# Performance work log

Measured on AMD Instinct MI355X. Metric: run time of the kernel, lower is better.

## Reference

```python
import jax, jax.numpy as jnp
import numpy as np

B, T, W_IN = 64, 512, 40
KS = 3
N = KS * KS          # 9 sampling points
CF = 8               # conv filters
GH = 32              # GRU hidden
GIN = (W_IN - KS + 1) * CF  # 304
ATTN = 32


def setup_inputs() -> dict:
    key = jax.random.key(0)
    ks = jax.random.split(key, 10)
    p = {}
    p["x"] = jax.random.normal(ks[0], (B, 1, T, W_IN), jnp.float32)
    p["p_w"] = jax.random.normal(ks[1], (2 * N, 1, KS, KS), jnp.float32) * 0.01
    p["p_b"] = jnp.zeros((2 * N,), jnp.float32)
    p["dcn_w"] = jax.random.normal(ks[2], (CF, 1, KS, KS), jnp.float32) * 0.1
    p["dcn_b"] = jnp.zeros((CF,), jnp.float32)
    p["w_ih"] = jax.random.normal(ks[3], (3 * GH, GIN), jnp.float32) * 0.05
    p["w_hh"] = jax.random.normal(ks[4], (3 * GH, GH), jnp.float32) * 0.05
    p["b_ih"] = jnp.zeros((3 * GH,), jnp.float32)
    p["b_hh"] = jnp.zeros((3 * GH,), jnp.float32)
    p["w1"] = jax.random.normal(ks[5], (ATTN, GH), jnp.float32) * 0.1
    p["b1"] = jnp.zeros((ATTN,), jnp.float32)
    p["w2"] = jax.random.normal(ks[6], (GH, ATTN), jnp.float32) * 0.1
    p["b2"] = jnp.zeros((GH,), jnp.float32)
    p["w3"] = jax.random.normal(ks[7], (2, GH), jnp.float32) * 0.1
    p["b3"] = jnp.zeros((2,), jnp.float32)
    return p


def _deform_conv(x, p_w, p_b, w, b):
    # x: (B,1,H,W). Deform-conv v1: offsets from a VALID 3x3 conv, bilinear gather.
    Bb, C, H, W = x.shape
    offset = jax.lax.conv_general_dilated(
        x, p_w, (1, 1), "VALID",
        dimension_numbers=("NCHW", "OIHW", "NCHW")) + p_b[None, :, None, None]
    h, w_ = offset.shape[2], offset.shape[3]  # (T-2, 38)
    r = KS // 2
    pny, pnx = jnp.meshgrid(jnp.arange(-r, r + 1), jnp.arange(-r, r + 1), indexing="ij")
    p0y, p0x = jnp.meshgrid(jnp.arange(1, h + 1), jnp.arange(1, w_ + 1), indexing="ij")
    py = offset[:, :N] + pny.reshape(1, N, 1, 1) + p0y[None, None]  # (B,N,h,w)
    px = offset[:, N:] + pnx.reshape(1, N, 1, 1) + p0x[None, None]
    py = jnp.clip(py, 0.0, H - 1.0)
    px = jnp.clip(px, 0.0, W - 1.0)
    y0 = jnp.floor(py).astype(jnp.int32)
    x0 = jnp.floor(px).astype(jnp.int32)
    y1 = jnp.minimum(y0 + 1, H - 1)
    x1 = jnp.minimum(x0 + 1, W - 1)
    wy = (py - y0)[:, None]  # (B,1,N,h,w)
    wx = (px - x0)[:, None]
    flat = x.reshape(Bb, C, H * W)

    def gather(yi, xi):
        idx = (yi * W + xi).reshape(Bb, 1, -1)
        g = jnp.take_along_axis(flat, idx, axis=2)
        return g.reshape(Bb, C, N, h, w_)

    g00 = gather(y0, x0); g01 = gather(y0, x1)
    g10 = gather(y1, x0); g11 = gather(y1, x1)
    samp = (g00 * (1 - wy) * (1 - wx) + g01 * (1 - wy) * wx
            + g10 * wy * (1 - wx) + g11 * wy * wx)  # (B,C,N,h,w)
    out = jnp.einsum("bcnhw,ocn->bohw", samp, w.reshape(w.shape[0], C, N))
    return out + b[None, :, None, None]


def _gru(seq, w_ih, w_hh, b_ih, b_hh):
    # seq: (T,B,GIN); PyTorch GRU equations, single layer, h0 = 0
    xp = jnp.einsum("tbi,hi->tbh", seq, w_ih) + b_ih  # (T,B,3H)
    h0 = jnp.zeros((seq.shape[1], GH), seq.dtype)

    def step(hprev, xt):
        hp = hprev @ w_hh.T + b_hh
        xr, xz, xn = jnp.split(xt, 3, axis=-1)
        hr, hz, hn = jnp.split(hp, 3, axis=-1)
        rg = jax.nn.sigmoid(xr + hr)
        zg = jax.nn.sigmoid(xz + hz)
        ng = jnp.tanh(xn + rg * hn)
        hnew = (1 - zg) * ng + zg * hprev
        return hnew, hnew

    _, ys = jax.lax.scan(step, h0, xp)
    return ys  # (T,B,GH)


def _forward(x, p_w, p_b, dcn_w, dcn_b, w_ih, w_hh, b_ih, b_hh, w1, b1, w2, b2, w3, b3):
    y = _deform_conv(x, p_w, p_b, dcn_w, dcn_b)        # (B,CF,h,w)
    h = y.shape[2]
    y = jnp.transpose(y, (2, 0, 3, 1)).reshape(h, y.shape[1], -1)  # wait
    return y


def _model(x, p_w, p_b, dcn_w, dcn_b, w_ih, w_hh, b_ih, b_hh, w1, b1, w2, b2, w3, b3):
    y = _deform_conv(x, p_w, p_b, dcn_w, dcn_b)        # (B,CF,h,w)
    Bb = y.shape[0]
    h = y.shape[2]
    seq = jnp.transpose(y, (2, 0, 3, 1)).reshape(h, Bb, -1)  # (h,B,w*CF) w-major then channel
    enc = jnp.transpose(_gru(seq, w_ih, w_hh, b_ih, b_hh), (1, 0, 2))  # (B,h,GH)
    a = jnp.tanh(enc @ w1.T + b1) @ w2.T + b2          # (B,h,GH)
    a = jax.nn.softmax(a, axis=1)                      # softmax over time
    pooled = jnp.sum(a * enc, axis=1)                  # (B,GH)
    return pooled @ w3.T + b3                          # (B,2)


def reference(x, p_w, p_b, dcn_w, dcn_b, w_ih, w_hh, b_ih, b_hh, w1, b1, w2, b2, w3, b3):
    return _model(x, p_w, p_b, dcn_w, dcn_b, w_ih, w_hh, b_ih, b_hh, w1, b1, w2, b2, w3, b3)
```

## Files before the change

kernel.cpp:

```cpp
#include <hip/hip_runtime.h>
#include <math.h>
#include <stdint.h>

#define BB 64
#define TT 512
#define W_IN 40
#define CF 8
#define GH 32
#define HOUT 510
#define WOUT 38
#define GIN 304
#define G3 96
#define ATT 32
#define MROWS (HOUT * BB)
#define KC2 152
#define WI_C 19

#define LOG2E 1.4426950408889634f

__device__ __forceinline__ float fast_rcp(float x) {
#if defined(__has_builtin)
# if __has_builtin(__builtin_amdgcn_rcpf)
    return __builtin_amdgcn_rcpf(x);
# else
    return 1.f / x;
# endif
#else
    return 1.f / x;
#endif
}

__device__ __forceinline__ float fast_exp2(float x) {
#if defined(__has_builtin)
# if __has_builtin(__builtin_amdgcn_exp2f)
    return __builtin_amdgcn_exp2f(x);
# else
    return exp2f(x);
# endif
#else
    return exp2f(x);
#endif
}

typedef __attribute__((address_space(3))) uint32_t lds_u32_t;
typedef const __attribute__((address_space(1))) uint32_t glb_u32_t;

__global__ __launch_bounds__(192, 1) void k_dcn_gemm(
    const float* __restrict__ x, const float* __restrict__ p_w, const float* __restrict__ p_b,
    const float* __restrict__ dcn_w, const float* __restrict__ dcn_b,
    const float* __restrict__ w_ih, const float* __restrict__ b_ih,
    float* __restrict__ xp)
{
    __shared__ float As[128 * KC2];
    __shared__ float Ws[96 * KC2];
    __shared__ float pw_s[162], pb_s[18], dw_s[72], db_s[8];

    const int tid = threadIdx.x;
    const int t0  = blockIdx.x * 2;
    const int r0  = blockIdx.x * 128;
    const int mg  = tid / 12;
    const int ng  = tid % 12;

    if (tid < 162) pw_s[tid] = p_w[tid];
    if (tid < 18)  pb_s[tid] = p_b[tid];
    if (tid < 72)  dw_s[tid] = dcn_w[tid];
    if (tid < 8)   db_s[tid] = dcn_b[tid];

    float bih[8];
    #pragma unroll
    for (int j = 0; j < 8; ++j) bih[j] = b_ih[ng + 12 * j];

    float acc[8][8];
    #pragma unroll
    for (int i = 0; i < 8; ++i)
        #pragma unroll
        for (int j = 0; j < 8; ++j) acc[i][j] = 0.f;

    auto stageW = [&](int ch) {
        for (int u4 = tid; u4 < 96 * (KC2 / 4); u4 += 192) {
            const int g   = u4 / (KC2 / 4);
            const int k4l = u4 % (KC2 / 4);
            const float* src = w_ih + (size_t)g * GIN + ch * KC2 + k4l * 4;
            float* dst = &Ws[u4 * 4];
#if defined(__has_builtin) && __has_builtin(__builtin_amdgcn_global_load_lds)
            __builtin_amdgcn_global_load_lds((glb_u32_t*)(uintptr_t)src,
                                             (lds_u32_t*)(uintptr_t)dst, 16, 0, 0);
#else
            *(float4*)dst = *(const float4*)src;
#endif
        }
    };

    auto phaseA = [&](int ch) {
        for (int item = tid; item < 128 * WI_C; item += 192) {
            const int lr = item / WI_C;
            const int wl = item % WI_C;
            const int wi = ch * WI_C + wl;
            const int t  = t0 + (lr >> 6);
            const int b  = lr & 63;
            const float* xb = x + (size_t)b * TT * W_IN;

            float patch[9];
            #pragma unroll
            for (int ky = 0; ky < 3; ++ky)
                #pragma unroll
                for (int kx = 0; kx < 3; ++kx)
                    patch[ky * 3 + kx] = xb[(t + ky) * W_IN + wi + kx];

            float offs[18];
            #pragma unroll
            for (int n = 0; n < 18; ++n) {
                float a = pb_s[n];
                #pragma unroll
                for (int k = 0; k < 9; ++k) a += patch[k] * pw_s[n * 9 + k];
                offs[n] = a;
            }

            float samp[9];
            #pragma unroll
            for (int n = 0; n < 9; ++n) {
                float py = offs[n]     + (float)(n / 3 - 1) + (float)(t + 1);
                float px = offs[9 + n] + (float)(n % 3 - 1) + (float)(wi + 1);
                py = fminf(fmaxf(py, 0.f), (float)(TT - 1));
                px = fminf(fmaxf(px, 0.f), (float)(W_IN - 1));
                float fy = floorf(py), fx = floorf(px);
                int y0 = (int)fy, x0 = (int)fx;
                int y1 = min(y0 + 1, TT - 1), x1 = min(x0 + 1, W_IN - 1);
                float wy = py - fy, wx = px - fx;
                float g00 = xb[y0 * W_IN + x0], g01 = xb[y0 * W_IN + x1];
                float g10 = xb[y1 * W_IN + x0], g11 = xb[y1 * W_IN + x1];
                samp[n] = g00 * (1.f - wy) * (1.f - wx) + g01 * (1.f - wy) * wx
                        + g10 * wy * (1.f - wx) + g11 * wy * wx;
            }

            float o[CF];
            #pragma unroll
            for (int c = 0; c < CF; ++c) {
                float a = db_s[c];
                #pragma unroll
                for (int n = 0; n < 9; ++n) a += samp[n] * dw_s[c * 9 + n];
                o[c] = a;
            }
            float* arow = &As[lr * KC2 + wl * 8];
            ((float4*)arow)[0] = make_float4(o[0], o[1], o[2], o[3]);
            ((float4*)arow)[1] = make_float4(o[4], o[5], o[6], o[7]);
        }
    };

    auto gemm = [&]() {
        #pragma unroll 2
        for (int k4 = 0; k4 < KC2 / 4; ++k4) {
            float4 a[8], w[8];
            #pragma unroll
            for (int i = 0; i < 8; ++i)
                a[i] = *(const float4*)&As[(mg + 16 * i) * KC2 + k4 * 4];
            #pragma unroll
            for (int j = 0; j < 8; ++j)
                w[j] = *(const float4*)&Ws[(ng + 12 * j) * KC2 + k4 * 4];
            #pragma unroll
            for (int i = 0; i < 8; ++i)
                #pragma unroll
                for (int j = 0; j < 8; ++j)
                    acc[i][j] += a[i].x * w[j].x + a[i].y * w[j].y
                               + a[i].z * w[j].z + a[i].w * w[j].w;
        }
    };

    __syncthreads();
    stageW(0);
    phaseA(0);
    __syncthreads();
    gemm();
    __syncthreads();
    stageW(1);
    phaseA(1);
    __syncthreads();
    gemm();

    #pragma unroll
    for (int i = 0; i < 8; ++i) {
        const int row = r0 + mg + 16 * i;
        #pragma unroll
        for (int j = 0; j < 8; ++j)
            xp[(size_t)row * G3 + ng + 12 * j] = acc[i][j] + bih[j];
    }
}

__global__ __launch_bounds__(64) void k_gru(
    const float* __restrict__ xp, const float* __restrict__ w_hh,
    const float* __restrict__ b_hh, float* __restrict__ enc)
{
    const int l = threadIdx.x;
    const int half = l >> 5;
    const int j = l & 31;
    const int b = blockIdx.x;

    float wr[16], wz[16], wn[16];
    #pragma unroll
    for (int i = 0; i < 16; ++i) {
        wr[i] = w_hh[(size_t)j * GH + half * 16 + i];
        wz[i] = w_hh[(size_t)(GH + j) * GH + half * 16 + i];
        wn[i] = w_hh[(size_t)(2 * GH + j) * GH + half * 16 + i];
    }
    const float br = b_hh[j], bz = b_hh[GH + j], bn = b_hh[2 * GH + j];

    float h = 0.f;
    const float* xb = xp + (size_t)b * G3;
    float xr = xb[j], xz = xb[GH + j], xn = xb[2 * GH + j];

    for (int t = 0; t < HOUT; ++t) {
        const int tn = (t + 1 < HOUT) ? t + 1 : t;
        const float* xq = xp + ((size_t)tn * BB + b) * G3;
        float nxr = xq[j], nxz = xq[GH + j], nxn = xq[2 * GH + j];

        float pr = 0.f, pz = 0.f, pn = 0.f;
        #pragma unroll
        for (int i = 0; i < 16; ++i) {
            float hk = __shfl(h, half * 16 + i, 64);
            pr += wr[i] * hk; pz += wz[i] * hk; pn += wn[i] * hk;
        }
        float ar = br + pr + __shfl_xor(pr, 32, 64);
        float az = bz + pz + __shfl_xor(pz, 32, 64);
        float an = bn + pn + __shfl_xor(pn, 32, 64);

        float rg = fast_rcp(1.f + fast_exp2(-(xr + ar) * LOG2E));
        float zg = fast_rcp(1.f + fast_exp2(-(xz + az) * LOG2E));
        float pre = xn + rg * an;
        float e2 = fast_exp2(pre * (2.f * LOG2E));
        float tg = 1.f - 2.f * fast_rcp(e2 + 1.f);
        h = (1.f - zg) * tg + zg * h;

        if (!half) enc[((size_t)b * HOUT + t) * GH + j] = h;
        xr = nxr; xz = nxz; xn = nxn;
    }
}

__global__ __launch_bounds__(256) void k_attn_part(
    const float* __restrict__ enc,
    const float* __restrict__ w1, const float* __restrict__ b1,
    const float* __restrict__ w2, const float* __restrict__ b2,
    float* __restrict__ part)
{
    __shared__ float w1s[ATT * 33], w2s[GH * 33];
    __shared__ float b1s[ATT], b2s[GH];
    __shared__ float encs[8][GH], apres[8][ATT];
    __shared__ float rm[8 * GH], rs[8 * GH], rp[8 * GH];

    const int b   = blockIdx.x >> 2;
    const int c   = blockIdx.x & 3;
    const int tid = threadIdx.x;
    const int ttl = tid >> 5;
    const int j   = tid & 31;

    for (int i = tid; i < ATT * GH; i += 256) {
        int r = i >> 5, cc = i & 31;
        w1s[r * 33 + cc] = w1[i];
        w2s[r * 33 + cc] = w2[i];
    }
    if (tid < ATT)           b1s[tid] = b1[tid];
    else if (tid < ATT + GH) b2s[tid - ATT] = b2[tid - ATT];
    __syncthreads();

    const int tbeg = c * 128;
    const int tend = min(HOUT, tbeg + 128);

    float m = -INFINITY, s = 0.f, p = 0.f;
    const float* encb = enc + (size_t)b * HOUT * GH;

    for (int t0 = tbeg; t0 < tend; t0 += 8) {
        const int t = t0 + ttl;
        const bool act = (t < tend);
        const float ev = act ? encb[t * GH + j] : 0.f;
        encs[ttl][j] = ev;
        __syncthreads();

        float a1 = b1s[j];
        #pragma unroll
        for (int k = 0; k < GH; ++k) a1 += encs[ttl][k] * w1s[j * 33 + k];
        apres[ttl][j] = tanhf(a1);
        __syncthreads();

        float a2 = b2s[j];
        #pragma unroll
        for (int k = 0; k < ATT; ++k) a2 += apres[ttl][k] * w2s[j * 33 + k];

        if (act) {
            float mn = fmaxf(m, a2);
            float sc = expf(m - mn);
            float e  = expf(a2 - mn);
            s = s * sc + e;
            p = p * sc + e * ev;
            m = mn;
        }
        __syncthreads();
    }

    rm[tid] = m; rs[tid] = s; rp[tid] = p;
    __syncthreads();

    if (tid < GH) {
        float M = -INFINITY;
        #pragma unroll
        for (int q = 0; q < 8; ++q) M = fmaxf(M, rm[q * GH + tid]);
        float S = 0.f, P = 0.f;
        #pragma unroll
        for (int q = 0; q < 8; ++q) {
            float sc = expf(rm[q * GH + tid] - M);
            S += rs[q * GH + tid] * sc;
            P += rp[q * GH + tid] * sc;
        }
        float* pb = part + ((size_t)b * 4 + c) * 96;
        pb[tid] = M; pb[32 + tid] = S; pb[64 + tid] = P;
    }
}

__global__ __launch_bounds__(64) void k_attn_fin(
    const float* __restrict__ part,
    const float* __restrict__ w3, const float* __restrict__ b3,
    float* __restrict__ out)
{
    __shared__ float pooled[GH];
    const int b = blockIdx.x;
    const int tid = threadIdx.x;

    if (tid < GH) {
        const float* pb = part + (size_t)b * 4 * 96;
        float M = -INFINITY;
        #pragma unroll
        for (int c = 0; c < 4; ++c) M = fmaxf(M, pb[c * 96 + tid]);
        float S = 0.f, P = 0.f;
        #pragma unroll
        for (int c = 0; c < 4; ++c) {
            float sc = expf(pb[c * 96 + tid] - M);
            S += pb[c * 96 + 32 + tid] * sc;
            P += pb[c * 96 + 64 + tid] * sc;
        }
        pooled[tid] = P / S;
    }
    __syncthreads();

    if (tid < 2) {
        float a = b3[tid];
        #pragma unroll
        for (int k = 0; k < GH; ++k) a += pooled[k] * w3[tid * GH + k];
        out[b * 2 + tid] = a;
    }
}

extern "C" void kernel_launch(void* const* d_in, const int* in_sizes, int n_in,
                              void* d_out, int out_size, void* d_ws, size_t ws_size,
                              hipStream_t stream)
{
    const float* x     = (const float*)d_in[0];
    const float* p_w   = (const float*)d_in[1];
    const float* p_b   = (const float*)d_in[2];
    const float* dcn_w = (const float*)d_in[3];
    const float* dcn_b = (const float*)d_in[4];
    const float* w_ih  = (const float*)d_in[5];
    const float* w_hh  = (const float*)d_in[6];
    const float* b_ih  = (const float*)d_in[7];
    const float* b_hh  = (const float*)d_in[8];
    const float* w1    = (const float*)d_in[9];
    const float* b1    = (const float*)d_in[10];
    const float* w2    = (const float*)d_in[11];
    const float* b2    = (const float*)d_in[12];
    const float* w3    = (const float*)d_in[13];
    const float* b3    = (const float*)d_in[14];
    float* out = (float*)d_out;

    float* xp   = (float*)d_ws;
    float* enc  = xp + (size_t)MROWS * G3;
    float* part = xp;

    hipLaunchKernelGGL(k_dcn_gemm, dim3(MROWS / 128), dim3(192), 0, stream,
                       x, p_w, p_b, dcn_w, dcn_b, w_ih, b_ih, xp);
    hipLaunchKernelGGL(k_gru, dim3(BB), dim3(64), 0, stream,
                       xp, w_hh, b_hh, enc);
    hipLaunchKernelGGL(k_attn_part, dim3(BB * 4), dim3(256), 0, stream,
                       enc, w1, b1, w2, b2, part);
    hipLaunchKernelGGL(k_attn_fin, dim3(BB), dim3(64), 0, stream,
                       part, w3, b3, out);
}
```

Baseline: 464.9 us.

## Double-buffer GRU input projections in LDS and split recurrent accumulators

The sequential GRU kernel now prefetches input projections for 16 timesteps at a time into a double-buffered LDS tile, using async global-to-LDS loads gated by explicit vmcnt waits. This replaces the per-step register prefetch of the next timestep. The 16-term recurrent dot products are also split into four partial accumulators to shorten the serial FMA dependency chain. The hand-written waitcnt counting assumes a single wave and a fixed number of outstanding loads, which makes it fragile.

```diff
diff --git a/kernel.cpp b/kernel.cpp
--- a/kernel.cpp
+++ b/kernel.cpp
@@ -13,8 +13,6 @@
 #define G3 96
 #define ATT 32
 #define MROWS (HOUT * BB)
-#define KC2 152
-#define WI_C 19
 
 #define LOG2E 1.4426950408889634f
 
@@ -45,7 +43,15 @@
 typedef __attribute__((address_space(3))) uint32_t lds_u32_t;
 typedef const __attribute__((address_space(1))) uint32_t glb_u32_t;
 
-__global__ __launch_bounds__(192, 1) void k_dcn_gemm(
+#if defined(__has_builtin) && __has_builtin(__builtin_amdgcn_global_load_lds)
+#define HAS_GLL 1
+#else
+#define HAS_GLL 0
+#endif
+
+#define KC2 152
+#define WI_C 19
+__global__ __launch_bounds__(192, 1) void k_dcn_gemm_fused(
     const float* __restrict__ x, const float* __restrict__ p_w, const float* __restrict__ p_b,
     const float* __restrict__ dcn_w, const float* __restrict__ dcn_b,
     const float* __restrict__ w_ih, const float* __restrict__ b_ih,
@@ -82,7 +88,7 @@
             const int k4l = u4 % (KC2 / 4);
             const float* src = w_ih + (size_t)g * GIN + ch * KC2 + k4l * 4;
             float* dst = &Ws[u4 * 4];
-#if defined(__has_builtin) && __has_builtin(__builtin_amdgcn_global_load_lds)
+#if HAS_GLL
             __builtin_amdgcn_global_load_lds((glb_u32_t*)(uintptr_t)src,
                                              (lds_u32_t*)(uintptr_t)dst, 16, 0, 0);
 #else
@@ -186,10 +192,15 @@
     }
 }
 
+#define GCH 16
+#define NCH 32
+
 __global__ __launch_bounds__(64) void k_gru(
     const float* __restrict__ xp, const float* __restrict__ w_hh,
     const float* __restrict__ b_hh, float* __restrict__ enc)
 {
+    __shared__ float xs[2][GCH * G3];
+
     const int l = threadIdx.x;
     const int half = l >> 5;
     const int j = l & 31;
@@ -204,34 +215,76 @@
     }
     const float br = b_hh[j], bz = b_hh[GH + j], bn = b_hh[2 * GH + j];
 
+    auto stage = [&](int c, int buf) {
+        #pragma unroll
+        for (int k = 0; k < 6; ++k) {
+            const int f  = k * 256 + l * 4;
+            const int tl = f / 96;
+            const int g  = f % 96;
+            int gt = c * GCH + tl;
+            if (gt > HOUT - 1) gt = HOUT - 1;
+            const float* src = xp + ((size_t)gt * BB + b) * G3 + g;
+            float* dst = &xs[buf][k * 256];
+#if HAS_GLL
+            __builtin_amdgcn_global_load_lds((glb_u32_t*)(uintptr_t)src,
+                                             (lds_u32_t*)(uintptr_t)dst, 16, 0, 0);
+#else
+            *(float4*)(&xs[buf][f]) = *(const float4*)src;
+#endif
+        }
+    };
+
+    stage(0, 0);
     float h = 0.f;
-    const float* xb = xp + (size_t)b * G3;
-    float xr = xb[j], xz = xb[GH + j], xn = xb[2 * GH + j];
-
-    for (int t = 0; t < HOUT; ++t) {
-        const int tn = (t + 1 < HOUT) ? t + 1 : t;
-        const float* xq = xp + ((size_t)tn * BB + b) * G3;
-        float nxr = xq[j], nxz = xq[GH + j], nxn = xq[2 * GH + j];
-
-        float pr = 0.f, pz = 0.f, pn = 0.f;
-        #pragma unroll
-        for (int i = 0; i < 16; ++i) {
-            float hk = __shfl(h, half * 16 + i, 64);
-            pr += wr[i] * hk; pz += wz[i] * hk; pn += wn[i] * hk;
-        }
-        float ar = br + pr + __shfl_xor(pr, 32, 64);
-        float az = bz + pz + __shfl_xor(pz, 32, 64);
-        float an = bn + pn + __shfl_xor(pn, 32, 64);
-
-        float rg = fast_rcp(1.f + fast_exp2(-(xr + ar) * LOG2E));
-        float zg = fast_rcp(1.f + fast_exp2(-(xz + az) * LOG2E));
-        float pre = xn + rg * an;
-        float e2 = fast_exp2(pre * (2.f * LOG2E));
-        float tg = 1.f - 2.f * fast_rcp(e2 + 1.f);
-        h = (1.f - zg) * tg + zg * h;
-
-        if (!half) enc[((size_t)b * HOUT + t) * GH + j] = h;
-        xr = nxr; xz = nxz; xn = nxn;
+
+    #pragma unroll 1
+    for (int c = 0; c < NCH; ++c) {
+        const int buf = c & 1;
+        if (c + 1 < NCH) {
+            stage(c + 1, buf ^ 1);
+            asm volatile("s_waitcnt vmcnt(6)" ::: "memory");
+        } else {
+            asm volatile("s_waitcnt vmcnt(0)" ::: "memory");
+        }
+        const int nst = (c == NCH - 1) ? (HOUT - (NCH - 1) * GCH) : GCH;
+        #pragma unroll 1
+        for (int tl = 0; tl < nst; ++tl) {
+            const float* xrow = &xs[buf][tl * G3];
+            const float xr = xrow[j], xz = xrow[GH + j], xn = xrow[2 * GH + j];
+
+            float pr0 = 0.f, pr1 = 0.f, pr2 = 0.f, pr3 = 0.f;
+            float pz0 = 0.f, pz1 = 0.f, pz2 = 0.f, pz3 = 0.f;
+            float pn0 = 0.f, pn1 = 0.f, pn2 = 0.f, pn3 = 0.f;
+            #pragma unroll
+            for (int i = 0; i < 16; i += 4) {
+                const float h0 = __shfl(h, half * 16 + i + 0, 64);
+                const float h1 = __shfl(h, half * 16 + i + 1, 64);
+                const float h2 = __shfl(h, half * 16 + i + 2, 64);
+                const float h3 = __shfl(h, half * 16 + i + 3, 64);
+                pr0 += wr[i + 0] * h0; pr1 += wr[i + 1] * h1;
+                pr2 += wr[i + 2] * h2; pr3 += wr[i + 3] * h3;
+                pz0 += wz[i + 0] * h0; pz1 += wz[i + 1] * h1;
+                pz2 += wz[i + 2] * h2; pz3 += wz[i + 3] * h3;
+                pn0 += wn[i + 0] * h0; pn1 += wn[i + 1] * h1;
+                pn2 += wn[i + 2] * h2; pn3 += wn[i + 3] * h3;
+            }
+            const float pr = (pr0 + pr1) + (pr2 + pr3);
+            const float pz = (pz0 + pz1) + (pz2 + pz3);
+            const float pn = (pn0 + pn1) + (pn2 + pn3);
+            const float ar = br + pr + __shfl_xor(pr, 32, 64);
+            const float az = bz + pz + __shfl_xor(pz, 32, 64);
+            const float an = bn + pn + __shfl_xor(pn, 32, 64);
+
+            const float rg = fast_rcp(1.f + fast_exp2(-(xr + ar) * LOG2E));
+            const float zg = fast_rcp(1.f + fast_exp2(-(xz + az) * LOG2E));
+            const float pre = xn + rg * an;
+            const float e2 = fast_exp2(pre * (2.f * LOG2E));
+            const float tg = 1.f - 2.f * fast_rcp(e2 + 1.f);
+            h = (1.f - zg) * tg + zg * h;
+
+            const int t = c * GCH + tl;
+            if (!half) enc[((size_t)b * HOUT + t) * GH + j] = h;
+        }
     }
 }
 
@@ -368,11 +421,12 @@
     const float* b3    = (const float*)d_in[14];
     float* out = (float*)d_out;
 
+    const size_t XP_F = (size_t)MROWS * G3;
     float* xp   = (float*)d_ws;
-    float* enc  = xp + (size_t)MROWS * G3;
+    float* enc  = xp + XP_F;
     float* part = xp;
 
-    hipLaunchKernelGGL(k_dcn_gemm, dim3(MROWS / 128), dim3(192), 0, stream,
+    hipLaunchKernelGGL(k_dcn_gemm_fused, dim3(MROWS / 128), dim3(192), 0, stream,
                        x, p_w, p_b, dcn_w, dcn_b, w_ih, b_ih, xp);
     hipLaunchKernelGGL(k_gru, dim3(BB), dim3(64), 0, stream,
                        xp, w_hh, b_hh, enc);
```

Measured after the change: 380.4 us. 18.2% less time.
